# Performance work log

Measured on AMD Instinct MI355X. Metric: run time of the kernel, lower is better.

The kernel has to match this reference:

```python
import jax, jax.numpy as jnp
import numpy as np

B = 512          # batch
H = 1024         # lstm hidden size
L = 2            # lstm layers
T = 144          # max_length
INPUT_SIZE = 16  # activity vocab
OUTPUT_SIZE = 17 # acts logits (16) + duration (1)
COND = 32        # conditionals_size
COND_H = 512     # conditional_hidden_size
ENC = H - COND_H # encoding_size = 512
EMB = ENC - 1    # embedding dim (concat with duration scalar -> ENC)


def setup_inputs() -> dict:
    key = jax.random.key(0)
    ks = jax.random.split(key, 16)
    s = 0.02
    return {
        "batch_size": B,
        "h0": jax.random.normal(ks[0], (L, B, H), jnp.float32) * s,
        "c0": jax.random.normal(ks[1], (L, B, H), jnp.float32) * s,
        "conditionals": jax.random.normal(ks[2], (B, COND), jnp.float32),
        "target_acts": jax.random.randint(ks[3], (B, T), 0, INPUT_SIZE),
        "target_durs": jax.random.uniform(ks[4], (B, T), jnp.float32),
        "emb_table": jax.random.normal(ks[5], (INPUT_SIZE, EMB), jnp.float32) * s,
        "ff_W": jax.random.normal(ks[6], (COND_H, COND), jnp.float32) * s,
        "ff_b": jnp.zeros((COND_H,), jnp.float32),
        "Wih": jax.random.normal(ks[7], (L, 4 * H, H), jnp.float32) * s,
        "Whh": jax.random.normal(ks[8], (L, 4 * H, H), jnp.float32) * s,
        "bih": jnp.zeros((L, 4 * H), jnp.float32),
        "bhh": jnp.zeros((L, 4 * H), jnp.float32),
        "fc_W": jax.random.normal(ks[9], (OUTPUT_SIZE, H), jnp.float32) * s,
        "fc_b": jnp.zeros((OUTPUT_SIZE,), jnp.float32),
    }


def reference(batch_size, h0, c0, conditionals, target_acts, target_durs,
              emb_table, ff_W, ff_b, Wih, Whh, bih, bhh, fc_W, fc_b):
    # conditional projection, injected at every step input: [B, COND_H]
    cond_h = conditionals @ ff_W.T + ff_b

    # teacher forcing: step 0 sees SOS (act=0, dur=0); step j>=1 sees target[:, j-1]
    acts_in = jnp.concatenate(
        [jnp.zeros((B, 1), target_acts.dtype), target_acts[:, :-1]], axis=1).T  # [T, B]
    durs_in = jnp.concatenate(
        [jnp.zeros((B, 1), target_durs.dtype), target_durs[:, :-1]], axis=1).T  # [T, B]

    def step(carry, xin):
        h, c = carry                      # each [L, B, H]
        act, dur = xin                    # [B], [B]
        emb = emb_table[act]              # [B, EMB]
        # CustomDurationEmbeddingConcat: concat(embed(act), dur) -> ENC, then concat cond -> H
        x = jnp.concatenate([emb, dur[:, None], cond_h], axis=-1)  # [B, H]
        hs, cs = [], []
        for l in range(L):
            gates = x @ Wih[l].T + h[l] @ Whh[l].T + bih[l] + bhh[l]  # [B, 4H]
            i, f, g, o = jnp.split(gates, 4, axis=-1)  # PyTorch gate order i,f,g,o
            cl = jax.nn.sigmoid(f) * c[l] + jax.nn.sigmoid(i) * jnp.tanh(g)
            hl = jax.nn.sigmoid(o) * jnp.tanh(cl)
            hs.append(hl)
            cs.append(cl)
            x = hl
        pred = x @ fc_W.T + fc_b          # [B, OUTPUT_SIZE]
        return (jnp.stack(hs), jnp.stack(cs)), pred

    _, preds = jax.lax.scan(step, (h0, c0), (acts_in, durs_in))  # preds [T, B, OUT]
    out = preds.transpose(1, 0, 2)                               # [B, T, OUT]
    logits = out[..., : OUTPUT_SIZE - 1]
    dur = out[..., OUTPUT_SIZE - 1:]
    # log-softmax over activity logits; log(sigmoid(dur)) for durations
    return jnp.concatenate(
        [jax.nn.log_softmax(logits, axis=-1), jax.nn.log_sigmoid(dur)], axis=-1)
```

## Files before the change

### kernel.cpp

```cpp
#include <hip/hip_runtime.h>
#include <hip/hip_bf16.h>
#include <stdint.h>

#define B_   512
#define H_   1024
#define T_   144
#define NG   4096
#define NOUT 17

typedef __bf16 bf16_t;
typedef __bf16 bf16x8 __attribute__((ext_vector_type(8)));
typedef float  f32x4  __attribute__((ext_vector_type(4)));

__device__ __host__ __forceinline__ int npack(int n) {
  int g = n >> 10, j = n & 1023;
  return ((j >> 4) << 6) + (g << 4) + (j & 15);
}
__device__ __forceinline__ float sigf(float x) { return 1.f / (1.f + __expf(-x)); }
__device__ __forceinline__ float tanhf_(float x) { return 1.f - 2.f / (__expf(2.f * x) + 1.f); }


__global__ void k_pack_wA(const float* __restrict__ Whh0, bf16_t* __restrict__ PB1) {
  int idx = blockIdx.x * 256 + threadIdx.x;
  int n = idx >> 7, kc = idx & 127;
  const float* s = Whh0 + (size_t)n * H_ + kc * 8;
  bf16x8 v;
#pragma unroll
  for (int e = 0; e < 8; ++e) v[e] = (bf16_t)s[e];
  int np = npack(n), jt = np >> 6, r = np & 63;
  *(bf16x8*)(PB1 + (size_t)jt * 65536 + (kc >> 2) * 2048 + r * 32 + (kc & 3) * 8) = v;
}

__global__ void k_pack_wB(const float* __restrict__ Wih1, const float* __restrict__ Whh1,
                          bf16_t* __restrict__ PB2) {
  int idx = blockIdx.x * 256 + threadIdx.x;
  int n = idx >> 8, kc = idx & 255;
  int k = kc * 8;
  const float* s = (k < H_) ? (Wih1 + (size_t)n * H_ + k) : (Whh1 + (size_t)n * H_ + (k - H_));
  bf16x8 v;
#pragma unroll
  for (int e = 0; e < 8; ++e) v[e] = (bf16_t)s[e];
  int np = npack(n), jt = np >> 6, r = np & 63;
  *(bf16x8*)(PB2 + (size_t)jt * 131072 + (kc >> 2) * 2048 + r * 32 + (kc & 3) * 8) = v;
}

__global__ void k_G(const float* __restrict__ Wih0, const float* __restrict__ ffW,
                    const float* __restrict__ ffb, float* __restrict__ G) {
  int n = blockIdx.x * 256 + threadIdx.x;
  float acc[33];
#pragma unroll
  for (int c = 0; c < 33; ++c) acc[c] = 0.f;
  for (int k = 0; k < 512; ++k) {
    float wv = Wih0[(size_t)n * H_ + 512 + k];
    const float* fr = ffW + (size_t)k * 32;
#pragma unroll
    for (int c = 0; c < 32; ++c) acc[c] += wv * fr[c];
    acc[32] += wv * ffb[k];
  }
  for (int c = 0; c < 33; ++c) G[(size_t)c * NG + n] = acc[c];
}

__global__ void k_CHp(const float* __restrict__ cond, const float* __restrict__ G,
                      const float* __restrict__ bih0, const float* __restrict__ bhh0,
                      float* __restrict__ CHp) {
  int idx = blockIdx.x * 256 + threadIdx.x;
  int b = idx >> 12, n = idx & 4095;
  float acc = bih0[n] + bhh0[n] + G[(size_t)32 * NG + n];
  const float* cb = cond + (size_t)b * 32;
#pragma unroll
  for (int c = 0; c < 32; ++c) acc += cb[c] * G[(size_t)c * NG + n];
  CHp[(size_t)b * NG + npack(n)] = acc;
}

__global__ void k_E16(const float* __restrict__ emb, const float* __restrict__ Wih0,
                      float* __restrict__ E16p) {
  int idx = blockIdx.x * 256 + threadIdx.x;
  int a = idx & 15, n = idx >> 4;
  const float* er = emb + (size_t)a * 511;
  const float* wr = Wih0 + (size_t)n * H_;
  float acc = 0.f;
  for (int k = 0; k < 511; ++k) acc += er[k] * wr[k];
  E16p[(size_t)a * NG + npack(n)] = acc;
}

__global__ void k_misc(const float* __restrict__ Wih0, const float* __restrict__ bih,
                       const float* __restrict__ bhh, const float* __restrict__ fcW,
                       bf16_t* __restrict__ fcWp, float* __restrict__ biasBp,
                       float* __restrict__ wcolp) {
  int idx = blockIdx.x * 256 + threadIdx.x;
  if (idx < NG) {
    int np = npack(idx);
    biasBp[np] = bih[NG + idx] + bhh[NG + idx];
    wcolp[np]  = Wih0[(size_t)idx * H_ + 511];
  }
  if (idx < 17 * H_) fcWp[idx] = (bf16_t)fcW[idx];
}

__global__ void k_init(const float* __restrict__ h0,
                       bf16_t* __restrict__ pah0i, bf16_t* __restrict__ pah1a) {
  int idx = blockIdx.x * 256 + threadIdx.x;
  int b = idx >> 7, kc = idx & 127;
  const float* s0 = h0 + (size_t)b * H_ + kc * 8;
  const float* s1 = s0 + (size_t)B_ * H_;
  bf16x8 v0, v1;
#pragma unroll
  for (int e = 0; e < 8; ++e) { v0[e] = (bf16_t)s0[e]; v1[e] = (bf16_t)s1[e]; }
  size_t po = (size_t)(kc >> 2) * 16384 + b * 32 + (kc & 3) * 8;
  *(bf16x8*)(pah0i + po) = v0;
  *(bf16x8*)(pah1a + po) = v1;
}


__global__ void k_out(const float* __restrict__ preds, const float* __restrict__ fcb,
                      float* __restrict__ out) {
  int idx = blockIdx.x * 256 + threadIdx.x;
  if (idx >= T_ * B_) return;
  int t = idx % T_, b = idx / T_;
  const float* pr = preds + ((size_t)t * B_ + b) * NOUT;
  float v[NOUT];
#pragma unroll
  for (int o = 0; o < NOUT; ++o) v[o] = pr[o] + fcb[o];
  float m = v[0];
#pragma unroll
  for (int o = 1; o < 16; ++o) m = fmaxf(m, v[o]);
  float s = 0.f;
#pragma unroll
  for (int o = 0; o < 16; ++o) s += expf(v[o] - m);
  float lse = m + logf(s);
  float* dst = out + ((size_t)b * T_ + t) * NOUT;
#pragma unroll
  for (int o = 0; o < 16; ++o) dst[o] = v[o] - lse;
  float x = v[16];
  dst[16] = (x > 0.f) ? -log1pf(expf(-x)) : (x - log1pf(expf(x)));
}


struct Params {
  const int* acts; const float* durs;
  const bf16_t* PB1; const bf16_t* PB2;
  const float* CHp; const float* E16p; const float* wcolp; const float* biasBp;
  const bf16_t* fcW;
  const float* c0in;
  const bf16_t* pah0i;
  bf16_t* pah0a; bf16_t* pah0b; bf16_t* pah1a; bf16_t* pah1b;
  unsigned* slots; float* preds;
};

__device__ __forceinline__ void gbar(unsigned* slots, unsigned phase, int tid, int wg) {
  __syncthreads();
  if (tid == 0) {
    __builtin_amdgcn_fence(__ATOMIC_RELEASE, "agent");
    __hip_atomic_store(slots + (size_t)wg * 16, phase, __ATOMIC_RELAXED, __HIP_MEMORY_SCOPE_AGENT);
  }
  if (tid < 64) {
#pragma unroll 1
    for (int j = 0; j < 4; ++j) {
      const unsigned* a = slots + (size_t)(tid + j * 64) * 16;
      while (__hip_atomic_load(a, __ATOMIC_RELAXED, __HIP_MEMORY_SCOPE_SYSTEM) < phase)
        __builtin_amdgcn_s_sleep(1);
    }
  }
  __syncthreads();
}

struct Slot { bf16x8 a0, a1, e0, e1, b0, b1, b2, b3, c0, c1, c2, c3, d0, d1, d2, d3; };

__device__ __forceinline__ void ldA(bf16x8& r0, bf16x8& r1, const char* p) {
  asm volatile("global_load_dwordx4 %0, %2, off sc0 sc1\n\t"
               "global_load_dwordx4 %1, %2, off offset:1024 sc0 sc1"
               : "=&v"(r0), "=&v"(r1) : "v"(p));
}
__device__ __forceinline__ void ldApl(bf16x8& r0, bf16x8& r1, const char* p) {
  asm volatile("global_load_dwordx4 %0, %2, off\n\t"
               "global_load_dwordx4 %1, %2, off offset:1024"
               : "=&v"(r0), "=&v"(r1) : "v"(p));
}
__device__ __forceinline__ void ldB4(bf16x8& r0, bf16x8& r1, bf16x8& r2, bf16x8& r3,
                                     const char* p) {
  asm volatile("global_load_dwordx4 %0, %4, off\n\t"
               "global_load_dwordx4 %1, %4, off offset:1024\n\t"
               "global_load_dwordx4 %2, %4, off offset:2048\n\t"
               "global_load_dwordx4 %3, %4, off offset:3072"
               : "=&v"(r0), "=&v"(r1), "=&v"(r2), "=&v"(r3) : "v"(p));
}

#define VMW(N) { asm volatile("s_waitcnt vmcnt(" #N ")" ::: "memory"); \
                 __builtin_amdgcn_sched_barrier(0); }

#define MFM(ACC, AV, BV) ACC = __builtin_amdgcn_mfma_f32_16x16x32_bf16(AV, BV, ACC, 0, 0, 0)

__device__ __forceinline__ void compS(f32x4 (&A0)[4][2], f32x4 (&A1)[4][2], const Slot& S) {
  MFM(A0[0][0], S.a0, S.b0); MFM(A0[0][1], S.a1, S.b0);
  MFM(A0[1][0], S.a0, S.b1); MFM(A0[1][1], S.a1, S.b1);
  MFM(A0[2][0], S.a0, S.b2); MFM(A0[2][1], S.a1, S.b2);
  MFM(A0[3][0], S.a0, S.b3); MFM(A0[3][1], S.a1, S.b3);
  MFM(A1[0][0], S.a0, S.c0); MFM(A1[0][1], S.a1, S.c0);
  MFM(A1[1][0], S.a0, S.c1); MFM(A1[1][1], S.a1, S.c1);
  MFM(A1[2][0], S.a0, S.c2); MFM(A1[2][1], S.a1, S.c2);
  MFM(A1[3][0], S.a0, S.c3); MFM(A1[3][1], S.a1, S.c3);
  MFM(A1[0][0], S.e0, S.d0); MFM(A1[0][1], S.e1, S.d0);
  MFM(A1[1][0], S.e0, S.d1); MFM(A1[1][1], S.e1, S.d1);
  MFM(A1[2][0], S.e0, S.d2); MFM(A1[2][1], S.e1, S.d2);
  MFM(A1[3][0], S.e0, S.d3); MFM(A1[3][1], S.e1, S.d3);
}

__device__ __forceinline__ void compP(f32x4 (&A0)[4][2], const Slot& S) {
  MFM(A0[0][0], S.a0, S.b0); MFM(A0[0][1], S.a1, S.b0);
  MFM(A0[1][0], S.a0, S.b1); MFM(A0[1][1], S.a1, S.b1);
  MFM(A0[2][0], S.a0, S.b2); MFM(A0[2][1], S.a1, S.b2);
  MFM(A0[3][0], S.a0, S.b3); MFM(A0[3][1], S.a1, S.b3);
}

__global__ __launch_bounds__(256, 1) void lstm_main(Params p) {
  const int tid = threadIdx.x;
  const int w = tid >> 6, l = tid & 63;
  const int wg = blockIdx.x;
  const int q = wg >> 3;
  const int mt = q & 3;
  const int jt = ((q >> 2) << 3) + (wg & 7);
  const int jj = l & 15, rq = l >> 4;
  const int jcol = jt * 16 + jj;
  const int npb = jt * 64;
  const int a_off = (w * 32 + jj) * 64 + rq * 16;
  const int b_off = jj * 64 + rq * 16;
  const char* Bw0 = (const char*)p.PB1 + (size_t)jt * 131072;
  const char* Bw1 = (const char*)p.PB2 + (size_t)jt * 262144;
  const int he_off = (jcol >> 5) * 16384 + (jcol & 31);

  float fcwf[16], fw16f[16];
  {
    const char* fwp = (const char*)p.fcW;
    bf16x8 fa = *(const bf16x8*)(fwp + jj * 2048 + jt * 32);
    bf16x8 fb = *(const bf16x8*)(fwp + jj * 2048 + jt * 32 + 16);
    bf16x8 ga = *(const bf16x8*)(fwp + 16 * 2048 + jt * 32);
    bf16x8 gb = *(const bf16x8*)(fwp + 16 * 2048 + jt * 32 + 16);
#pragma unroll
    for (int e = 0; e < 8; ++e) {
      fcwf[e] = (float)fa[e]; fcwf[8 + e] = (float)fb[e];
      fw16f[e] = (float)ga[e]; fw16f[8 + e] = (float)gb[e];
    }
  }

  float chv[2][4][4], cv0[2][4], cv1[2][4], bzv[4], wcv[4];
#pragma unroll
  for (int rg = 0; rg < 2; ++rg)
#pragma unroll
    for (int qq = 0; qq < 4; ++qq) {
      int b = mt * 128 + w * 32 + rg * 16 + rq * 4 + qq;
      cv0[rg][qq] = p.c0in[(size_t)b * H_ + jcol];
      cv1[rg][qq] = p.c0in[(size_t)B_ * H_ + (size_t)b * H_ + jcol];
#pragma unroll
      for (int g = 0; g < 4; ++g)
        chv[rg][qq][g] = p.CHp[(size_t)b * NG + npb + g * 16 + jj];
    }
#pragma unroll
  for (int g = 0; g < 4; ++g) {
    bzv[g] = p.biasBp[npb + g * 16 + jj];
    wcv[g] = p.wcolp[npb + g * 16 + jj];
  }

  Slot S0, S1, S2;

  {
    f32x4 acc0[4][2];
#pragma unroll
    for (int g = 0; g < 4; ++g)
#pragma unroll
      for (int rg = 0; rg < 2; ++rg) acc0[g][rg] = (f32x4){0.f, 0.f, 0.f, 0.f};

    const char* Ai = (const char*)p.pah0i;
    auto Pp = [&](int kk, Slot& S) {
      ldApl(S.a0, S.a1, Ai + (size_t)kk * 32768 + a_off);
      ldB4(S.b0, S.b1, S.b2, S.b3, Bw0 + (size_t)kk * 4096 + b_off);
    };
    Pp(0, S0); Pp(1, S1);
#pragma unroll 1
    for (int o = 0; o < 10; ++o) {
      const int k = o * 3;
      Pp(k + 2, S2); VMW(12); compP(acc0, S0);
      Pp(k + 3, S0); VMW(12); compP(acc0, S1);
      Pp(k + 4, S1); VMW(12); compP(acc0, S2);
    }
    VMW(6);  compP(acc0, S0);
    VMW(0);  compP(acc0, S1);

    bf16_t* H0n = p.pah0a;
#pragma unroll
    for (int rg = 0; rg < 2; ++rg)
#pragma unroll
      for (int qq = 0; qq < 4; ++qq) {
        int b = mt * 128 + w * 32 + rg * 16 + rq * 4 + qq;
        float pre[4];
#pragma unroll
        for (int g = 0; g < 4; ++g)
          pre[g] = acc0[g][rg][qq] + chv[rg][qq][g] + p.E16p[npb + g * 16 + jj];
        float cn = sigf(pre[1]) * cv0[rg][qq] + sigf(pre[0]) * tanhf_(pre[2]);
        float hn = sigf(pre[3]) * tanhf_(cn);
        cv0[rg][qq] = cn;
        H0n[(size_t)he_off + b * 32] = (bf16_t)hn;
      }
    gbar(p.slots, 1u, tid, wg);
  }

#pragma unroll 1
  for (int s = 0; s < T_; ++s) {
    const char* Ah0 = (const char*)((s & 1) ? p.pah0b : p.pah0a);
    bf16_t*     H0n = (s & 1) ? p.pah0a : p.pah0b;
    const char* Ah1 = (const char*)((s & 1) ? p.pah1b : p.pah1a);
    bf16_t*     H1n = (s & 1) ? p.pah1a : p.pah1b;

    f32x4 acc0[4][2], acc1[4][2];
#pragma unroll
    for (int g = 0; g < 4; ++g)
#pragma unroll
      for (int rg = 0; rg < 2; ++rg) {
        acc0[g][rg] = (f32x4){0.f, 0.f, 0.f, 0.f};
        acc1[g][rg] = (f32x4){0.f, 0.f, 0.f, 0.f};
      }

    auto Pm = [&](int kk, Slot& S) {
      ldA(S.a0, S.a1, Ah0 + (size_t)kk * 32768 + a_off);
      ldA(S.e0, S.e1, Ah1 + (size_t)kk * 32768 + a_off);
      ldB4(S.b0, S.b1, S.b2, S.b3, Bw0 + (size_t)kk * 4096 + b_off);
      ldB4(S.c0, S.c1, S.c2, S.c3, Bw1 + (size_t)kk * 4096 + b_off);
      ldB4(S.d0, S.d1, S.d2, S.d3, Bw1 + (size_t)(32 + kk) * 4096 + b_off);
    };
    Pm(0, S0); Pm(1, S1);
#pragma unroll 1
    for (int o = 0; o < 10; ++o) {
      const int k = o * 3;
      Pm(k + 2, S2); VMW(32); compS(acc0, acc1, S0);
      Pm(k + 3, S0); VMW(32); compS(acc0, acc1, S1);
      Pm(k + 4, S1); VMW(32); compS(acc0, acc1, S2);
    }
    VMW(16); compS(acc0, acc1, S0);
    VMW(0);  compS(acc0, acc1, S1);

#pragma unroll
    for (int rg = 0; rg < 2; ++rg)
#pragma unroll
      for (int qq = 0; qq < 4; ++qq) {
        int b = mt * 128 + w * 32 + rg * 16 + rq * 4 + qq;
        float pre1[4];
#pragma unroll
        for (int g = 0; g < 4; ++g) pre1[g] = acc1[g][rg][qq] + bzv[g];
        float cn1 = sigf(pre1[1]) * cv1[rg][qq] + sigf(pre1[0]) * tanhf_(pre1[2]);
        float hn1 = sigf(pre1[3]) * tanhf_(cn1);
        cv1[rg][qq] = cn1;
        H1n[(size_t)he_off + b * 32] = (bf16_t)hn1;
        float accO = 0.f, acc16 = 0.f;
#pragma unroll
        for (int sc = 0; sc < 16; ++sc) {
          float hs = __shfl(hn1, (l & 48) | sc, 64);
          accO  += hs * fcwf[sc];
          acc16 += hs * fw16f[sc];
        }
        float* pb = p.preds + ((size_t)s * B_ + b) * NOUT;
        atomicAdd(pb + jj, accO);
        if (jj == 15) atomicAdd(pb + 16, acc16);
        int act = p.acts[(size_t)b * T_ + s];
        float dur = p.durs[(size_t)b * T_ + s];
        float pre0[4];
#pragma unroll
        for (int g = 0; g < 4; ++g)
          pre0[g] = acc0[g][rg][qq] + chv[rg][qq][g]
                  + p.E16p[(size_t)act * NG + npb + g * 16 + jj] + dur * wcv[g];
        float cn0 = sigf(pre0[1]) * cv0[rg][qq] + sigf(pre0[0]) * tanhf_(pre0[2]);
        float hn0 = sigf(pre0[3]) * tanhf_(cn0);
        cv0[rg][qq] = cn0;
        H0n[(size_t)he_off + b * 32] = (bf16_t)hn0;
      }
    gbar(p.slots, (unsigned)(s + 2), tid, wg);
  }
}


extern "C" void kernel_launch(void* const* d_in, const int* in_sizes, int n_in,
                              void* d_out, int out_size, void* d_ws, size_t ws_size,
                              hipStream_t stream) {
  (void)in_sizes; (void)n_in; (void)out_size; (void)ws_size;
  const float* h0   = (const float*)d_in[1];
  const float* c0   = (const float*)d_in[2];
  const float* cond = (const float*)d_in[3];
  const int*   acts = (const int*)d_in[4];
  const float* durs = (const float*)d_in[5];
  const float* emb  = (const float*)d_in[6];
  const float* ffW  = (const float*)d_in[7];
  const float* ffb  = (const float*)d_in[8];
  const float* Wih  = (const float*)d_in[9];
  const float* Whh  = (const float*)d_in[10];
  const float* bih  = (const float*)d_in[11];
  const float* bhh  = (const float*)d_in[12];
  const float* fcW  = (const float*)d_in[13];
  const float* fcb  = (const float*)d_in[14];

  char* ws = (char*)d_ws;
  size_t off = 0;
  auto alloc = [&](size_t bytes) -> char* {
    char* p0 = ws + off;
    off = (off + bytes + 255) & ~(size_t)255;
    return p0;
  };
  unsigned* slots = (unsigned*)alloc(256 * 64);
  bf16_t* PB1     = (bf16_t*)alloc((size_t)NG * H_ * 2);
  bf16_t* PB2     = (bf16_t*)alloc((size_t)NG * 2048 * 2);
  float*  CHp     = (float*)alloc((size_t)B_ * NG * 4);
  float*  E16p    = (float*)alloc((size_t)16 * NG * 4);
  float*  wcolp   = (float*)alloc((size_t)NG * 4);
  float*  biasBp  = (float*)alloc((size_t)NG * 4);
  float*  G       = (float*)alloc((size_t)33 * NG * 4);
  bf16_t* fcWp    = (bf16_t*)alloc((size_t)17 * H_ * 2);
  bf16_t* pah0i   = (bf16_t*)alloc((size_t)B_ * H_ * 2);
  bf16_t* pah0a   = (bf16_t*)alloc((size_t)B_ * H_ * 2);
  bf16_t* pah0b   = (bf16_t*)alloc((size_t)B_ * H_ * 2);
  bf16_t* pah1a   = (bf16_t*)alloc((size_t)B_ * H_ * 2);
  bf16_t* pah1b   = (bf16_t*)alloc((size_t)B_ * H_ * 2);
  float*  preds   = (float*)alloc((size_t)T_ * B_ * NOUT * 4);

  hipMemsetAsync(slots, 0, 256 * 64, stream);
  hipMemsetAsync(preds, 0, (size_t)T_ * B_ * NOUT * 4, stream);
  k_pack_wA<<<2048, 256, 0, stream>>>(Whh, PB1);
  k_pack_wB<<<4096, 256, 0, stream>>>(Wih + (size_t)NG * H_, Whh + (size_t)NG * H_, PB2);
  k_G<<<16, 256, 0, stream>>>(Wih, ffW, ffb, G);
  k_CHp<<<8192, 256, 0, stream>>>(cond, G, bih, bhh, CHp);
  k_E16<<<256, 256, 0, stream>>>(emb, Wih, E16p);
  k_misc<<<68, 256, 0, stream>>>(Wih, bih, bhh, fcW, fcWp, biasBp, wcolp);
  k_init<<<256, 256, 0, stream>>>(h0, pah0i, pah1a);

  Params prm;
  prm.acts = acts; prm.durs = durs;
  prm.PB1 = PB1; prm.PB2 = PB2;
  prm.CHp = CHp; prm.E16p = E16p; prm.wcolp = wcolp; prm.biasBp = biasBp;
  prm.fcW = fcWp;
  prm.c0in = c0;
  prm.pah0i = pah0i;
  prm.pah0a = pah0a; prm.pah0b = pah0b; prm.pah1a = pah1a; prm.pah1b = pah1b;
  prm.slots = slots; prm.preds = preds;

  lstm_main<<<dim3(256), dim3(256), 0, stream>>>(prm);
  k_out<<<(T_ * B_ + 255) / 256, 256, 0, stream>>>(preds, fcb, (float*)d_out);
}
```

Baseline: 7.302 ms.

## Split persistent LSTM kernel across 512 workgroups with halved batch tile

Doubles the persistent grid from 256 to 512 workgroups, each handling 64 batch rows instead of 128, so each wave keeps one 16-row A fragment and half the accumulators. Register use drops (chv moved to per-step global loads, fc weights kept packed as bf16), allowing two workgroups per CU via launch bounds. The global barrier now polls 512 slots using all threads. This raises parallelism and latency hiding but doubles weight-tile reads across workgroups and makes the grid barrier larger.

```diff
diff --git a/kernel.cpp b/kernel.cpp
--- a/kernel.cpp
+++ b/kernel.cpp
@@ -152,28 +152,24 @@
     __builtin_amdgcn_fence(__ATOMIC_RELEASE, "agent");
     __hip_atomic_store(slots + (size_t)wg * 16, phase, __ATOMIC_RELAXED, __HIP_MEMORY_SCOPE_AGENT);
   }
-  if (tid < 64) {
-#pragma unroll 1
-    for (int j = 0; j < 4; ++j) {
-      const unsigned* a = slots + (size_t)(tid + j * 64) * 16;
-      while (__hip_atomic_load(a, __ATOMIC_RELAXED, __HIP_MEMORY_SCOPE_SYSTEM) < phase)
-        __builtin_amdgcn_s_sleep(1);
-    }
+  {
+    const unsigned* a0 = slots + (size_t)tid * 16;
+    const unsigned* a1 = slots + (size_t)(tid + 256) * 16;
+    while (__hip_atomic_load(a0, __ATOMIC_RELAXED, __HIP_MEMORY_SCOPE_SYSTEM) < phase)
+      __builtin_amdgcn_s_sleep(1);
+    while (__hip_atomic_load(a1, __ATOMIC_RELAXED, __HIP_MEMORY_SCOPE_SYSTEM) < phase)
+      __builtin_amdgcn_s_sleep(1);
   }
   __syncthreads();
 }
 
-struct Slot { bf16x8 a0, a1, e0, e1, b0, b1, b2, b3, c0, c1, c2, c3, d0, d1, d2, d3; };
-
-__device__ __forceinline__ void ldA(bf16x8& r0, bf16x8& r1, const char* p) {
-  asm volatile("global_load_dwordx4 %0, %2, off sc0 sc1\n\t"
-               "global_load_dwordx4 %1, %2, off offset:1024 sc0 sc1"
-               : "=&v"(r0), "=&v"(r1) : "v"(p));
-}
-__device__ __forceinline__ void ldApl(bf16x8& r0, bf16x8& r1, const char* p) {
-  asm volatile("global_load_dwordx4 %0, %2, off\n\t"
-               "global_load_dwordx4 %1, %2, off offset:1024"
-               : "=&v"(r0), "=&v"(r1) : "v"(p));
+struct Slot { bf16x8 a0, e0, b0, b1, b2, b3, c0, c1, c2, c3, d0, d1, d2, d3; };
+
+__device__ __forceinline__ void ldA1(bf16x8& r0, const char* p) {
+  asm volatile("global_load_dwordx4 %0, %1, off sc0 sc1" : "=&v"(r0) : "v"(p));
+}
+__device__ __forceinline__ void ldA1pl(bf16x8& r0, const char* p) {
+  asm volatile("global_load_dwordx4 %0, %1, off" : "=&v"(r0) : "v"(p));
 }
 __device__ __forceinline__ void ldB4(bf16x8& r0, bf16x8& r1, bf16x8& r2, bf16x8& r3,
                                      const char* p) {
@@ -189,70 +185,51 @@
 
 #define MFM(ACC, AV, BV) ACC = __builtin_amdgcn_mfma_f32_16x16x32_bf16(AV, BV, ACC, 0, 0, 0)
 
-__device__ __forceinline__ void compS(f32x4 (&A0)[4][2], f32x4 (&A1)[4][2], const Slot& S) {
-  MFM(A0[0][0], S.a0, S.b0); MFM(A0[0][1], S.a1, S.b0);
-  MFM(A0[1][0], S.a0, S.b1); MFM(A0[1][1], S.a1, S.b1);
-  MFM(A0[2][0], S.a0, S.b2); MFM(A0[2][1], S.a1, S.b2);
-  MFM(A0[3][0], S.a0, S.b3); MFM(A0[3][1], S.a1, S.b3);
-  MFM(A1[0][0], S.a0, S.c0); MFM(A1[0][1], S.a1, S.c0);
-  MFM(A1[1][0], S.a0, S.c1); MFM(A1[1][1], S.a1, S.c1);
-  MFM(A1[2][0], S.a0, S.c2); MFM(A1[2][1], S.a1, S.c2);
-  MFM(A1[3][0], S.a0, S.c3); MFM(A1[3][1], S.a1, S.c3);
-  MFM(A1[0][0], S.e0, S.d0); MFM(A1[0][1], S.e1, S.d0);
-  MFM(A1[1][0], S.e0, S.d1); MFM(A1[1][1], S.e1, S.d1);
-  MFM(A1[2][0], S.e0, S.d2); MFM(A1[2][1], S.e1, S.d2);
-  MFM(A1[3][0], S.e0, S.d3); MFM(A1[3][1], S.e1, S.d3);
-}
-
-__device__ __forceinline__ void compP(f32x4 (&A0)[4][2], const Slot& S) {
-  MFM(A0[0][0], S.a0, S.b0); MFM(A0[0][1], S.a1, S.b0);
-  MFM(A0[1][0], S.a0, S.b1); MFM(A0[1][1], S.a1, S.b1);
-  MFM(A0[2][0], S.a0, S.b2); MFM(A0[2][1], S.a1, S.b2);
-  MFM(A0[3][0], S.a0, S.b3); MFM(A0[3][1], S.a1, S.b3);
-}
-
-__global__ __launch_bounds__(256, 1) void lstm_main(Params p) {
+__device__ __forceinline__ void compS(f32x4 (&A0)[4], f32x4 (&A1)[4], const Slot& S) {
+  MFM(A0[0], S.a0, S.b0); MFM(A0[1], S.a0, S.b1);
+  MFM(A0[2], S.a0, S.b2); MFM(A0[3], S.a0, S.b3);
+  MFM(A1[0], S.a0, S.c0); MFM(A1[1], S.a0, S.c1);
+  MFM(A1[2], S.a0, S.c2); MFM(A1[3], S.a0, S.c3);
+  MFM(A1[0], S.e0, S.d0); MFM(A1[1], S.e0, S.d1);
+  MFM(A1[2], S.e0, S.d2); MFM(A1[3], S.e0, S.d3);
+}
+
+__device__ __forceinline__ void compP(f32x4 (&A0)[4], const Slot& S) {
+  MFM(A0[0], S.a0, S.b0); MFM(A0[1], S.a0, S.b1);
+  MFM(A0[2], S.a0, S.b2); MFM(A0[3], S.a0, S.b3);
+}
+
+__global__ __launch_bounds__(256, 2) void lstm_main(Params p) {
   const int tid = threadIdx.x;
   const int w = tid >> 6, l = tid & 63;
   const int wg = blockIdx.x;
-  const int q = wg >> 3;
-  const int mt = q & 3;
-  const int jt = ((q >> 2) << 3) + (wg & 7);
+  const int mt2 = (wg >> 3) & 7;
+  const int jt = ((wg >> 6) << 3) | (wg & 7);
   const int jj = l & 15, rq = l >> 4;
   const int jcol = jt * 16 + jj;
   const int npb = jt * 64;
-  const int a_off = (w * 32 + jj) * 64 + rq * 16;
+  const int a_off = (mt2 * 64 + w * 16 + jj) * 64 + rq * 16;
   const int b_off = jj * 64 + rq * 16;
   const char* Bw0 = (const char*)p.PB1 + (size_t)jt * 131072;
   const char* Bw1 = (const char*)p.PB2 + (size_t)jt * 262144;
   const int he_off = (jcol >> 5) * 16384 + (jcol & 31);
 
-  float fcwf[16], fw16f[16];
+  bf16x8 fcw_a, fcw_b, fw16_a, fw16_b;
   {
     const char* fwp = (const char*)p.fcW;
-    bf16x8 fa = *(const bf16x8*)(fwp + jj * 2048 + jt * 32);
-    bf16x8 fb = *(const bf16x8*)(fwp + jj * 2048 + jt * 32 + 16);
-    bf16x8 ga = *(const bf16x8*)(fwp + 16 * 2048 + jt * 32);
-    bf16x8 gb = *(const bf16x8*)(fwp + 16 * 2048 + jt * 32 + 16);
-#pragma unroll
-    for (int e = 0; e < 8; ++e) {
-      fcwf[e] = (float)fa[e]; fcwf[8 + e] = (float)fb[e];
-      fw16f[e] = (float)ga[e]; fw16f[8 + e] = (float)gb[e];
-    }
-  }
-
-  float chv[2][4][4], cv0[2][4], cv1[2][4], bzv[4], wcv[4];
-#pragma unroll
-  for (int rg = 0; rg < 2; ++rg)
-#pragma unroll
-    for (int qq = 0; qq < 4; ++qq) {
-      int b = mt * 128 + w * 32 + rg * 16 + rq * 4 + qq;
-      cv0[rg][qq] = p.c0in[(size_t)b * H_ + jcol];
-      cv1[rg][qq] = p.c0in[(size_t)B_ * H_ + (size_t)b * H_ + jcol];
-#pragma unroll
-      for (int g = 0; g < 4; ++g)
-        chv[rg][qq][g] = p.CHp[(size_t)b * NG + npb + g * 16 + jj];
-    }
+    fcw_a  = *(const bf16x8*)(fwp + jj * 2048 + jt * 32);
+    fcw_b  = *(const bf16x8*)(fwp + jj * 2048 + jt * 32 + 16);
+    fw16_a = *(const bf16x8*)(fwp + 16 * 2048 + jt * 32);
+    fw16_b = *(const bf16x8*)(fwp + 16 * 2048 + jt * 32 + 16);
+  }
+
+  float cv0[4], cv1[4], bzv[4], wcv[4];
+#pragma unroll
+  for (int qq = 0; qq < 4; ++qq) {
+    int b = mt2 * 64 + w * 16 + rq * 4 + qq;
+    cv0[qq] = p.c0in[(size_t)b * H_ + jcol];
+    cv1[qq] = p.c0in[(size_t)B_ * H_ + (size_t)b * H_ + jcol];
+  }
 #pragma unroll
   for (int g = 0; g < 4; ++g) {
     bzv[g] = p.biasBp[npb + g * 16 + jj];
@@ -262,43 +239,40 @@
   Slot S0, S1, S2;
 
   {
-    f32x4 acc0[4][2];
-#pragma unroll
-    for (int g = 0; g < 4; ++g)
-#pragma unroll
-      for (int rg = 0; rg < 2; ++rg) acc0[g][rg] = (f32x4){0.f, 0.f, 0.f, 0.f};
+    f32x4 acc0[4];
+#pragma unroll
+    for (int g = 0; g < 4; ++g) acc0[g] = (f32x4){0.f, 0.f, 0.f, 0.f};
 
     const char* Ai = (const char*)p.pah0i;
     auto Pp = [&](int kk, Slot& S) {
-      ldApl(S.a0, S.a1, Ai + (size_t)kk * 32768 + a_off);
+      ldA1pl(S.a0, Ai + (size_t)kk * 32768 + a_off);
       ldB4(S.b0, S.b1, S.b2, S.b3, Bw0 + (size_t)kk * 4096 + b_off);
     };
     Pp(0, S0); Pp(1, S1);
 #pragma unroll 1
     for (int o = 0; o < 10; ++o) {
       const int k = o * 3;
-      Pp(k + 2, S2); VMW(12); compP(acc0, S0);
-      Pp(k + 3, S0); VMW(12); compP(acc0, S1);
-      Pp(k + 4, S1); VMW(12); compP(acc0, S2);
+      Pp(k + 2, S2); VMW(10); compP(acc0, S0);
+      Pp(k + 3, S0); VMW(10); compP(acc0, S1);
+      Pp(k + 4, S1); VMW(10); compP(acc0, S2);
     }
-    VMW(6);  compP(acc0, S0);
+    VMW(5);  compP(acc0, S0);
     VMW(0);  compP(acc0, S1);
 
     bf16_t* H0n = p.pah0a;
 #pragma unroll
-    for (int rg = 0; rg < 2; ++rg)
-#pragma unroll
-      for (int qq = 0; qq < 4; ++qq) {
-        int b = mt * 128 + w * 32 + rg * 16 + rq * 4 + qq;
-        float pre[4];
-#pragma unroll
-        for (int g = 0; g < 4; ++g)
-          pre[g] = acc0[g][rg][qq] + chv[rg][qq][g] + p.E16p[npb + g * 16 + jj];
-        float cn = sigf(pre[1]) * cv0[rg][qq] + sigf(pre[0]) * tanhf_(pre[2]);
-        float hn = sigf(pre[3]) * tanhf_(cn);
-        cv0[rg][qq] = cn;
-        H0n[(size_t)he_off + b * 32] = (bf16_t)hn;
-      }
+    for (int qq = 0; qq < 4; ++qq) {
+      int b = mt2 * 64 + w * 16 + rq * 4 + qq;
+      float pre[4];
+#pragma unroll
+      for (int g = 0; g < 4; ++g)
+        pre[g] = acc0[g][qq] + p.CHp[(size_t)b * NG + npb + g * 16 + jj]
+               + p.E16p[npb + g * 16 + jj];
+      float cn = sigf(pre[1]) * cv0[qq] + sigf(pre[0]) * tanhf_(pre[2]);
+      float hn = sigf(pre[3]) * tanhf_(cn);
+      cv0[qq] = cn;
+      H0n[(size_t)he_off + b * 32] = (bf16_t)hn;
+    }
     gbar(p.slots, 1u, tid, wg);
   }
 
@@ -309,18 +283,16 @@
     const char* Ah1 = (const char*)((s & 1) ? p.pah1b : p.pah1a);
     bf16_t*     H1n = (s & 1) ? p.pah1a : p.pah1b;
 
-    f32x4 acc0[4][2], acc1[4][2];
-#pragma unroll
-    for (int g = 0; g < 4; ++g)
-#pragma unroll
-      for (int rg = 0; rg < 2; ++rg) {
-        acc0[g][rg] = (f32x4){0.f, 0.f, 0.f, 0.f};
-        acc1[g][rg] = (f32x4){0.f, 0.f, 0.f, 0.f};
-      }
+    f32x4 acc0[4], acc1[4];
+#pragma unroll
+    for (int g = 0; g < 4; ++g) {
+      acc0[g] = (f32x4){0.f, 0.f, 0.f, 0.f};
+      acc1[g] = (f32x4){0.f, 0.f, 0.f, 0.f};
+    }
 
     auto Pm = [&](int kk, Slot& S) {
-      ldA(S.a0, S.a1, Ah0 + (size_t)kk * 32768 + a_off);
-      ldA(S.e0, S.e1, Ah1 + (size_t)kk * 32768 + a_off);
+      ldA1(S.a0, Ah0 + (size_t)kk * 32768 + a_off);
+      ldA1(S.e0, Ah1 + (size_t)kk * 32768 + a_off);
       ldB4(S.b0, S.b1, S.b2, S.b3, Bw0 + (size_t)kk * 4096 + b_off);
       ldB4(S.c0, S.c1, S.c2, S.c3, Bw1 + (size_t)kk * 4096 + b_off);
       ldB4(S.d0, S.d1, S.d2, S.d3, Bw1 + (size_t)(32 + kk) * 4096 + b_off);
@@ -329,47 +301,51 @@
 #pragma unroll 1
     for (int o = 0; o < 10; ++o) {
       const int k = o * 3;
-      Pm(k + 2, S2); VMW(32); compS(acc0, acc1, S0);
-      Pm(k + 3, S0); VMW(32); compS(acc0, acc1, S1);
-      Pm(k + 4, S1); VMW(32); compS(acc0, acc1, S2);
+      Pm(k + 2, S2); VMW(28); compS(acc0, acc1, S0);
+      Pm(k + 3, S0); VMW(28); compS(acc0, acc1, S1);
+      Pm(k + 4, S1); VMW(28); compS(acc0, acc1, S2);
     }
-    VMW(16); compS(acc0, acc1, S0);
+    VMW(14); compS(acc0, acc1, S0);
     VMW(0);  compS(acc0, acc1, S1);
 
 #pragma unroll
-    for (int rg = 0; rg < 2; ++rg)
-#pragma unroll
-      for (int qq = 0; qq < 4; ++qq) {
-        int b = mt * 128 + w * 32 + rg * 16 + rq * 4 + qq;
-        float pre1[4];
-#pragma unroll
-        for (int g = 0; g < 4; ++g) pre1[g] = acc1[g][rg][qq] + bzv[g];
-        float cn1 = sigf(pre1[1]) * cv1[rg][qq] + sigf(pre1[0]) * tanhf_(pre1[2]);
-        float hn1 = sigf(pre1[3]) * tanhf_(cn1);
-        cv1[rg][qq] = cn1;
-        H1n[(size_t)he_off + b * 32] = (bf16_t)hn1;
-        float accO = 0.f, acc16 = 0.f;
-#pragma unroll
-        for (int sc = 0; sc < 16; ++sc) {
-          float hs = __shfl(hn1, (l & 48) | sc, 64);
-          accO  += hs * fcwf[sc];
-          acc16 += hs * fw16f[sc];
-        }
-        float* pb = p.preds + ((size_t)s * B_ + b) * NOUT;
-        atomicAdd(pb + jj, accO);
-        if (jj == 15) atomicAdd(pb + 16, acc16);
-        int act = p.acts[(size_t)b * T_ + s];
-        float dur = p.durs[(size_t)b * T_ + s];
-        float pre0[4];
-#pragma unroll
-        for (int g = 0; g < 4; ++g)
-          pre0[g] = acc0[g][rg][qq] + chv[rg][qq][g]
-                  + p.E16p[(size_t)act * NG + npb + g * 16 + jj] + dur * wcv[g];
-        float cn0 = sigf(pre0[1]) * cv0[rg][qq] + sigf(pre0[0]) * tanhf_(pre0[2]);
-        float hn0 = sigf(pre0[3]) * tanhf_(cn0);
-        cv0[rg][qq] = cn0;
-        H0n[(size_t)he_off + b * 32] = (bf16_t)hn0;
+    for (int qq = 0; qq < 4; ++qq) {
+      int b = mt2 * 64 + w * 16 + rq * 4 + qq;
+      float pre1[4];
+#pragma unroll
+      for (int g = 0; g < 4; ++g) pre1[g] = acc1[g][qq] + bzv[g];
+      float cn1 = sigf(pre1[1]) * cv1[qq] + sigf(pre1[0]) * tanhf_(pre1[2]);
+      float hn1 = sigf(pre1[3]) * tanhf_(cn1);
+      cv1[qq] = cn1;
+      H1n[(size_t)he_off + b * 32] = (bf16_t)hn1;
+      float accO = 0.f, acc16 = 0.f;
+#pragma unroll
+      for (int sc = 0; sc < 8; ++sc) {
+        float hs = __shfl(hn1, (l & 48) | sc, 64);
+        accO  += hs * (float)fcw_a[sc];
+        acc16 += hs * (float)fw16_a[sc];
       }
+#pragma unroll
+      for (int sc = 0; sc < 8; ++sc) {
+        float hs = __shfl(hn1, (l & 48) | (8 + sc), 64);
+        accO  += hs * (float)fcw_b[sc];
+        acc16 += hs * (float)fw16_b[sc];
+      }
+      float* pb = p.preds + ((size_t)s * B_ + b) * NOUT;
+      atomicAdd(pb + jj, accO);
+      if (jj == 15) atomicAdd(pb + 16, acc16);
+      int act = p.acts[(size_t)b * T_ + s];
+      float dur = p.durs[(size_t)b * T_ + s];
+      float pre0[4];
+#pragma unroll
+      for (int g = 0; g < 4; ++g)
+        pre0[g] = acc0[g][qq] + p.CHp[(size_t)b * NG + npb + g * 16 + jj]
+                + p.E16p[(size_t)act * NG + npb + g * 16 + jj] + dur * wcv[g];
+      float cn0 = sigf(pre0[1]) * cv0[qq] + sigf(pre0[0]) * tanhf_(pre0[2]);
+      float hn0 = sigf(pre0[3]) * tanhf_(cn0);
+      cv0[qq] = cn0;
+      H0n[(size_t)he_off + b * 32] = (bf16_t)hn0;
+    }
     gbar(p.slots, (unsigned)(s + 2), tid, wg);
   }
 }
@@ -401,7 +377,7 @@
     off = (off + bytes + 255) & ~(size_t)255;
     return p0;
   };
-  unsigned* slots = (unsigned*)alloc(256 * 64);
+  unsigned* slots = (unsigned*)alloc(512 * 64);
   bf16_t* PB1     = (bf16_t*)alloc((size_t)NG * H_ * 2);
   bf16_t* PB2     = (bf16_t*)alloc((size_t)NG * 2048 * 2);
   float*  CHp     = (float*)alloc((size_t)B_ * NG * 4);
@@ -417,7 +393,7 @@
   bf16_t* pah1b   = (bf16_t*)alloc((size_t)B_ * H_ * 2);
   float*  preds   = (float*)alloc((size_t)T_ * B_ * NOUT * 4);
 
-  hipMemsetAsync(slots, 0, 256 * 64, stream);
+  hipMemsetAsync(slots, 0, 512 * 64, stream);
   hipMemsetAsync(preds, 0, (size_t)T_ * B_ * NOUT * 4, stream);
   k_pack_wA<<<2048, 256, 0, stream>>>(Whh, PB1);
   k_pack_wB<<<4096, 256, 0, stream>>>(Wih + (size_t)NG * H_, Whh + (size_t)NG * H_, PB2);
@@ -437,6 +413,6 @@
   prm.pah0a = pah0a; prm.pah0b = pah0b; prm.pah1a = pah1a; prm.pah1b = pah1b;
   prm.slots = slots; prm.preds = preds;
 
-  lstm_main<<<dim3(256), dim3(256), 0, stream>>>(prm);
+  lstm_main<<<dim3(512), dim3(256), 0, stream>>>(prm);
   k_out<<<(T_ * B_ + 255) / 256, 256, 0, stream>>>(preds, fcb, (float*)d_out);
 }
```

Result: slower. 10.89 ms (+49.1%).
